# Optimization experiments

Hardware: AMD Instinct MI355X
Metric: run time of the kernel (lower is better)

Reference implementation:

```python
import jax, jax.numpy as jnp
import numpy as np

SIMPLE_W = 1.0
NON_SIMPLE_W = 5.0

# connectivity offset sets (exclude center)
_ALL26 = [(a, b, c) for a in (-1, 0, 1) for b in (-1, 0, 1) for c in (-1, 0, 1) if (a, b, c) != (0, 0, 0)]
OFF6 = [o for o in _ALL26 if abs(o[0]) + abs(o[1]) + abs(o[2]) == 1]          # scipy default structure
OFF18 = [o for o in _ALL26 if not (abs(o[0]) == 1 and abs(o[1]) == 1 and abs(o[2]) == 1)]  # the 's' structure
OFF26 = _ALL26                                                                  # np.ones((3,3,3))


def global_label(fg):
    """Connected-component labels (6-connectivity) via max-propagation.
    Labels are distinct positive ints per component (values differ from scipy's
    1..K but only label *equality* is used downstream). fg: bool [D,H,W]."""
    D, H, W = fg.shape
    idx = (jnp.arange(fg.size, dtype=jnp.int32) + 1).reshape(fg.shape)
    lab0 = jnp.where(fg, idx, 0)

    def step(lab):
        p = jnp.pad(lab, 1)
        m = lab
        for dz, dy, dx in OFF6:
            m = jnp.maximum(m, p[1 + dz:1 + dz + D, 1 + dy:1 + dy + H, 1 + dx:1 + dx + W])
        return jnp.where(fg, m, 0)

    def cond(c):
        return ~c[1]

    def body(c):
        lab, _ = c
        new = step(lab)
        return new, jnp.all(new == lab)

    lab, _ = jax.lax.while_loop(cond, body, (lab0, jnp.array(False)))
    return lab


def local_ncomp(mask, offsets):
    """Number of connected components inside each 3x3x3 window.
    mask: bool [N,3,3,3]. Max-propagation of unique seeds for 26 iters
    (>= max path length among 27 voxels); a component is counted where the
    surviving max label equals its own seed."""
    seed = (jnp.arange(27, dtype=jnp.int32) + 1).reshape(3, 3, 3)
    lab0 = jnp.where(mask, seed, 0)

    def body(_, lab):
        p = jnp.pad(lab, ((0, 0), (1, 1), (1, 1), (1, 1)))
        m = lab
        for dz, dy, dx in offsets:
            m = jnp.maximum(m, p[:, 1 + dz:4 + dz, 1 + dy:4 + dy, 1 + dx:4 + dx])
        return jnp.where(mask, m, 0)

    lab = jax.lax.fori_loop(0, 26, body, lab0)
    return jnp.sum((lab == seed) & mask, axis=(1, 2, 3))


def nonsimple_map(x):
    """Per-voxel non-simple-point indicator, float, same shape as x."""
    D, H, W = x.shape
    fg = x > 0
    glab = global_label(fg)
    p = jnp.pad(glab, 1, mode='edge')  # np.pad(..., 'edge')
    # 3x3x3 label windows per voxel -> [N,3,3,3]
    wins = jnp.stack([p[dz:dz + D, dy:dy + H, dx:dx + W]
                      for dz in range(3) for dy in range(3) for dx in range(3)], axis=-1)
    wins = wins.reshape(-1, 3, 3, 3)
    center = wins[:, 1, 1, 1]  # [N]
    c = center[:, None, None, None]
    # test 1: complement-of-center-label components (18-connectivity) must be exactly 1
    n1 = local_ncomp(wins != c, OFF18)
    # test 2: center-label components with center voxel removed (26-conn) must be exactly 1
    mask2 = (wins == c).at[:, 1, 1, 1].set(False)
    n2 = local_ncomp(mask2, OFF26)
    ns = (center != 0) & ((n1 != 1) | (n2 != 1))
    return ns.reshape(D, H, W).astype(x.dtype)


def setup_inputs() -> dict:
    key = jax.random.key(0)
    k1, k2 = jax.random.split(key)
    D = H = W = 64
    prediction = jax.random.normal(k1, (D, H, W), dtype=jnp.float32)
    label = jax.random.randint(k2, (D, H, W), 0, 2).astype(jnp.float32)
    return {"prediction": prediction, "label": label}


def reference(prediction, label):
    pw = nonsimple_map(prediction)
    lw = nonsimple_map(label)
    w_bool = (pw + lw) > 0
    weight = jnp.where(w_bool, NON_SIMPLE_W, SIMPLE_W).astype(prediction.dtype)
    # BCEWithLogitsLoss(reduction='none'): max(x,0) - x*y + log(1+exp(-|x|))
    cost = jnp.maximum(prediction, 0.0) - prediction * label + jnp.log1p(jnp.exp(-jnp.abs(prediction)))
    return jnp.mean(weight * cost)
```

## Files before the change

kernel.cpp:

```cpp
#include <hip/hip_runtime.h>

#define DIM 64
#define NVOX (DIM * DIM * DIM)

__device__ __forceinline__ int find_root_link(int* L, int v) {
    for (;;) {
        int p = L[v];
        if (p == v) return v;
        int gp = L[p];
        if (gp == p) return p;
        L[v] = gp;
        v = gp;
    }
}

__device__ __forceinline__ void unite(int* L, int a, int b) {
    int ra = find_root_link(L, a);
    int rb = find_root_link(L, b);
    while (ra != rb) {
        if (ra > rb) { int t = ra; ra = rb; rb = t; }
        int old = atomicCAS(&L[rb], rb, ra);
        if (old == rb) break;
        rb = find_root_link(L, old);
        ra = find_root_link(L, ra);
    }
}

__global__ void local_ccl(const float* __restrict__ pred,
                          const float* __restrict__ lab,
                          int* __restrict__ LP, int* __restrict__ LL) {
    __shared__ int s_lab[512];
    int t = threadIdx.x;
    int b = blockIdx.x;
    int tx = b & 3, ty = (b >> 2) & 7, tz = b >> 5;
    int lx = t & 15, ly = (t >> 4) & 7, lz = t >> 7;
    int x = (tx << 4) | lx, y = (ty << 3) | ly, z = (tz << 2) | lz;
    int v = (z << 12) | (y << 6) | x;

    const float* src = blockIdx.y ? lab : pred;
    int* Lg = blockIdx.y ? LL : LP;

    bool fg = src[v] > 0.0f;
    s_lab[t] = fg ? t : -1;
    __syncthreads();

    if (fg) {
        if (lx < 15 && s_lab[t + 1]   >= 0) unite(s_lab, t, t + 1);
        if (ly < 7  && s_lab[t + 16]  >= 0) unite(s_lab, t, t + 16);
        if (lz < 3  && s_lab[t + 128] >= 0) unite(s_lab, t, t + 128);
    }
    __syncthreads();

    int g = -1;
    if (fg) {
        int p = s_lab[t];
        while (s_lab[p] != p) p = s_lab[p];
        int rx = (tx << 4) | (p & 15);
        int ry = (ty << 3) | ((p >> 4) & 7);
        int rz = (tz << 2) | (p >> 7);
        g = (rz << 12) | (ry << 6) | rx;
    }
    Lg[v] = g;
}

__global__ void boundary_link(int* __restrict__ LP, int* __restrict__ LL) {
    int v = blockIdx.x * blockDim.x + threadIdx.x;
    int x = v & 63, y = (v >> 6) & 63, z = v >> 12;
    bool bx = ((x & 15) == 15) && (x != 63);
    bool by = ((y & 7)  == 7)  && (y != 63);
    bool bz = ((z & 3)  == 3)  && (z != 63);
    if (!(bx | by | bz)) return;
    if (LP[v] >= 0) {
        if (bx && LP[v + 1]    >= 0) unite(LP, v, v + 1);
        if (by && LP[v + 64]   >= 0) unite(LP, v, v + 64);
        if (bz && LP[v + 4096] >= 0) unite(LP, v, v + 4096);
    }
    if (LL[v] >= 0) {
        if (bx && LL[v + 1]    >= 0) unite(LL, v, v + 1);
        if (by && LL[v + 64]   >= 0) unite(LL, v, v + 64);
        if (bz && LL[v + 4096] >= 0) unite(LL, v, v + 4096);
    }
}

__global__ void compress_kernel(int* __restrict__ LP, int* __restrict__ LL) {
    int v = blockIdx.x * blockDim.x + threadIdx.x;
    int p = LP[v];
    if (p >= 0) { int q = LP[p]; while (q != p) { p = q; q = LP[p]; } LP[v] = p; }
    p = LL[v];
    if (p >= 0) { int q = LL[p]; while (q != p) { p = q; q = LL[p]; } LL[v] = p; }
}

#define MX_L 0x6DB6DB6u
#define MX_R 0x36DB6DBu
#define MY_L 0x7E3F1F8u
#define MY_R 0x0FC7E3Fu
#define M27  0x7FFFFFFu

__device__ __forceinline__ unsigned dil26(unsigned m) {
    m |= ((m << 1) & MX_L) | ((m >> 1) & MX_R);
    m |= ((m << 3) & MY_L) | ((m >> 3) & MY_R);
    m |= ((m << 9) & M27)  | (m >> 9);
    return m;
}
__device__ __forceinline__ unsigned dil18(unsigned m) {
    unsigned ax = m | ((m << 1) & MX_L) | ((m >> 1) & MX_R);
    unsigned ay = m | ((m << 3) & MY_L) | ((m >> 3) & MY_R);
    unsigned dxy = ax | ((ax << 3) & MY_L) | ((ax >> 3) & MY_R);
    unsigned dxz = ax | ((ax << 9) & M27)  | (ax >> 9);
    unsigned dyz = ay | ((ay << 9) & M27)  | (ay >> 9);
    return dxy | dxz | dyz;
}

__device__ __forceinline__ bool single18(unsigned m) {
    if (!m) return false;
    unsigned c = m & (~m + 1u);
    for (;;) {
        unsigned n = dil18(c) & m;
        if (n == m) return true;
        if (n == c) return false;
        c = n;
    }
}
__device__ __forceinline__ bool single26(unsigned m) {
    if (!m) return false;
    unsigned c = m & (~m + 1u);
    for (;;) {
        unsigned n = dil26(c) & m;
        if (n == m) return true;
        if (n == c) return false;
        c = n;
    }
}

#define HV 600

__global__ void finalize_kernel(const float* __restrict__ pred,
                                const float* __restrict__ lab,
                                const int* __restrict__ LP,
                                const int* __restrict__ LL,
                                float* __restrict__ out) {
    __shared__ int sP[HV], sL[HV];
    __shared__ float s_part[4];
    int t = threadIdx.x;
    int b = blockIdx.x;
    int tx = b & 7, ty = (b >> 3) & 7, tz = b >> 6;
    int x0 = tx << 3, y0 = ty << 3, z0 = tz << 2;

    for (int i = t; i < HV; i += 256) {
        int hx = i % 10, r = i / 10, hy = r % 10, hz = r / 10;
        int gx = x0 + hx - 1; gx = gx < 0 ? 0 : (gx > 63 ? 63 : gx);
        int gy = y0 + hy - 1; gy = gy < 0 ? 0 : (gy > 63 ? 63 : gy);
        int gz = z0 + hz - 1; gz = gz < 0 ? 0 : (gz > 63 ? 63 : gz);
        int gv = (gz << 12) | (gy << 6) | gx;
        sP[i] = LP[gv];
        sL[i] = LL[gv];
    }
    __syncthreads();

    int lx = t & 7, ly = (t >> 3) & 7, lz = t >> 6;
    int x = x0 | lx, y = y0 | ly, z = z0 | lz;
    int v = (z << 12) | (y << 6) | x;
    int base = lz * 100 + ly * 10 + lx;

    bool nsP = false, nsL = false;
    {
        int c = sP[base + 111];
        if (c >= 0) {
            unsigned m1 = 0, m2 = 0; int k = 0;
#pragma unroll
            for (int kz = 0; kz < 3; ++kz)
#pragma unroll
                for (int ky = 0; ky < 3; ++ky)
#pragma unroll
                    for (int kx = 0; kx < 3; ++kx, ++k) {
                        int w = sP[base + kz * 100 + ky * 10 + kx];
                        m1 |= (unsigned)(w != c) << k;
                        m2 |= (unsigned)(w == c) << k;
                    }
            m2 &= ~(1u << 13);
            nsP = !(single18(m1) && single26(m2));
        }
    }
    {
        int c = sL[base + 111];
        if (c >= 0) {
            unsigned m1 = 0, m2 = 0; int k = 0;
#pragma unroll
            for (int kz = 0; kz < 3; ++kz)
#pragma unroll
                for (int ky = 0; ky < 3; ++ky)
#pragma unroll
                    for (int kx = 0; kx < 3; ++kx, ++k) {
                        int w = sL[base + kz * 100 + ky * 10 + kx];
                        m1 |= (unsigned)(w != c) << k;
                        m2 |= (unsigned)(w == c) << k;
                    }
            m2 &= ~(1u << 13);
            nsL = !(single18(m1) && single26(m2));
        }
    }

    float p = pred[v], l = lab[v];
    float cost = fmaxf(p, 0.0f) - p * l + log1pf(__expf(-fabsf(p)));
    float w = (nsP || nsL) ? 5.0f : 1.0f;
    float contrib = w * cost;

#pragma unroll
    for (int off = 32; off > 0; off >>= 1)
        contrib += __shfl_down(contrib, off, 64);
    if ((t & 63) == 0) s_part[t >> 6] = contrib;
    __syncthreads();
    if (t == 0) {
        float s = s_part[0] + s_part[1] + s_part[2] + s_part[3];
        atomicAdd(out, s * (1.0f / (float)NVOX));
    }
}

extern "C" void kernel_launch(void* const* d_in, const int* in_sizes, int n_in,
                              void* d_out, int out_size, void* d_ws, size_t ws_size,
                              hipStream_t stream) {
    const float* pred = (const float*)d_in[0];
    const float* lab  = (const float*)d_in[1];
    float* out = (float*)d_out;

    int* LP = (int*)d_ws;
    int* LL = LP + NVOX;

    hipMemsetAsync(d_out, 0, sizeof(float), stream);

    hipLaunchKernelGGL(local_ccl, dim3(512, 2), dim3(512), 0, stream,
                       pred, lab, LP, LL);
    hipLaunchKernelGGL(boundary_link, dim3(NVOX / 256), dim3(256), 0, stream,
                       LP, LL);
    hipLaunchKernelGGL(compress_kernel, dim3(NVOX / 256), dim3(256), 0, stream,
                       LP, LL);
    hipLaunchKernelGGL(finalize_kernel, dim3(NVOX / 256), dim3(256), 0, stream,
                       pred, lab, LP, LL, out);
}
```

Baseline: 128.1 us.

## Enlarge CCL tiles, index boundary edges directly, fold root compression into finalize

Local CCL tiles grow from 16x8x4 to 16x16x8 voxels, with each thread handling 8 voxels, so far fewer inter-tile boundary edges remain. The boundary kernel now enumerates only the actual boundary face pairs, one edge per thread, instead of scanning every voxel and exiting early. The separate compress kernel is removed, and finalize chases each halo voxel's chain to its root while loading it. This cuts one launch and most idle boundary threads, but finalize now performs uncompressed pointer chasing for every halo element, which can be deep chains of global reads.

```diff
diff --git a/kernel.cpp b/kernel.cpp
--- a/kernel.cpp
+++ b/kernel.cpp
@@ -29,65 +29,79 @@
 __global__ void local_ccl(const float* __restrict__ pred,
                           const float* __restrict__ lab,
                           int* __restrict__ LP, int* __restrict__ LL) {
-    __shared__ int s_lab[512];
+    __shared__ int s_lab[2048];
     int t = threadIdx.x;
     int b = blockIdx.x;
-    int tx = b & 3, ty = (b >> 2) & 7, tz = b >> 5;
-    int lx = t & 15, ly = (t >> 4) & 7, lz = t >> 7;
-    int x = (tx << 4) | lx, y = (ty << 3) | ly, z = (tz << 2) | lz;
-    int v = (z << 12) | (y << 6) | x;
+    int tx = b & 3, ty = (b >> 2) & 3, tz = b >> 4;
+    int X0 = tx << 4, Y0 = ty << 4, Z0 = tz << 3;
 
     const float* src = blockIdx.y ? lab : pred;
     int* Lg = blockIdx.y ? LL : LP;
 
-    bool fg = src[v] > 0.0f;
-    s_lab[t] = fg ? t : -1;
-    __syncthreads();
-
-    if (fg) {
-        if (lx < 15 && s_lab[t + 1]   >= 0) unite(s_lab, t, t + 1);
-        if (ly < 7  && s_lab[t + 16]  >= 0) unite(s_lab, t, t + 16);
-        if (lz < 3  && s_lab[t + 128] >= 0) unite(s_lab, t, t + 128);
-    }
-    __syncthreads();
-
-    int g = -1;
-    if (fg) {
-        int p = s_lab[t];
-        while (s_lab[p] != p) p = s_lab[p];
-        int rx = (tx << 4) | (p & 15);
-        int ry = (ty << 3) | ((p >> 4) & 7);
-        int rz = (tz << 2) | (p >> 7);
-        g = (rz << 12) | (ry << 6) | rx;
-    }
-    Lg[v] = g;
-}
+    bool fg[8];
+    int vv[8];
+#pragma unroll
+    for (int i = 0; i < 8; ++i) {
+        int l = t + (i << 8);
+        int v = ((Z0 + (l >> 8)) << 12) | ((Y0 + ((l >> 4) & 15)) << 6)
+              | (X0 + (l & 15));
+        vv[i] = v;
+        fg[i] = src[v] > 0.0f;
+        s_lab[l] = fg[i] ? l : -1;
+    }
+    __syncthreads();
+
+#pragma unroll
+    for (int i = 0; i < 8; ++i) {
+        if (!fg[i]) continue;
+        int l = t + (i << 8);
+        int lx = l & 15, ly = (l >> 4) & 15, lz = l >> 8;
+        if (lx < 15 && s_lab[l + 1]   >= 0) unite(s_lab, l, l + 1);
+        if (ly < 15 && s_lab[l + 16]  >= 0) unite(s_lab, l, l + 16);
+        if (lz < 7  && s_lab[l + 256] >= 0) unite(s_lab, l, l + 256);
+    }
+    __syncthreads();
+
+#pragma unroll
+    for (int i = 0; i < 8; ++i) {
+        int g = -1;
+        if (fg[i]) {
+            int p = s_lab[t + (i << 8)];
+            while (s_lab[p] != p) p = s_lab[p];
+            g = ((Z0 + (p >> 8)) << 12) | ((Y0 + ((p >> 4) & 15)) << 6)
+              | (X0 + (p & 15));
+        }
+        Lg[vv[i]] = g;
+    }
+}
+
+#define EPF 53248
 
 __global__ void boundary_link(int* __restrict__ LP, int* __restrict__ LL) {
-    int v = blockIdx.x * blockDim.x + threadIdx.x;
-    int x = v & 63, y = (v >> 6) & 63, z = v >> 12;
-    bool bx = ((x & 15) == 15) && (x != 63);
-    bool by = ((y & 7)  == 7)  && (y != 63);
-    bool bz = ((z & 3)  == 3)  && (z != 63);
-    if (!(bx | by | bz)) return;
-    if (LP[v] >= 0) {
-        if (bx && LP[v + 1]    >= 0) unite(LP, v, v + 1);
-        if (by && LP[v + 64]   >= 0) unite(LP, v, v + 64);
-        if (bz && LP[v + 4096] >= 0) unite(LP, v, v + 4096);
-    }
-    if (LL[v] >= 0) {
-        if (bx && LL[v + 1]    >= 0) unite(LL, v, v + 1);
-        if (by && LL[v + 64]   >= 0) unite(LL, v, v + 64);
-        if (bz && LL[v + 4096] >= 0) unite(LL, v, v + 4096);
-    }
-}
-
-__global__ void compress_kernel(int* __restrict__ LP, int* __restrict__ LL) {
-    int v = blockIdx.x * blockDim.x + threadIdx.x;
-    int p = LP[v];
-    if (p >= 0) { int q = LP[p]; while (q != p) { p = q; q = LP[p]; } LP[v] = p; }
-    p = LL[v];
-    if (p >= 0) { int q = LL[p]; while (q != p) { p = q; q = LL[p]; } LL[v] = p; }
+    int e = blockIdx.x * blockDim.x + threadIdx.x;
+    int f = e >= EPF;
+    int r = f ? e - EPF : e;
+    int* L = f ? LL : LP;
+    int v, n;
+    if (r < 12288) {
+        int plane = 15 + ((r >> 12) << 4);
+        int ij = r & 4095;
+        v = ((ij >> 6) << 12) | ((ij & 63) << 6) | plane;
+        n = v + 1;
+    } else if (r < 24576) {
+        int r2 = r - 12288;
+        int plane = 15 + ((r2 >> 12) << 4);
+        int ij = r2 & 4095;
+        v = ((ij >> 6) << 12) | (plane << 6) | (ij & 63);
+        n = v + 64;
+    } else {
+        int r3 = r - 24576;
+        int plane = 7 + ((r3 >> 12) << 3);
+        int ij = r3 & 4095;
+        v = (plane << 12) | ((ij >> 6) << 6) | (ij & 63);
+        n = v + 4096;
+    }
+    if (L[v] >= 0 && L[n] >= 0) unite(L, v, n);
 }
 
 #define MX_L 0x6DB6DB6u
@@ -152,8 +166,12 @@
         int gy = y0 + hy - 1; gy = gy < 0 ? 0 : (gy > 63 ? 63 : gy);
         int gz = z0 + hz - 1; gz = gz < 0 ? 0 : (gz > 63 ? 63 : gz);
         int gv = (gz << 12) | (gy << 6) | gx;
-        sP[i] = LP[gv];
-        sL[i] = LL[gv];
+        int p = LP[gv];
+        if (p >= 0) { int q = LP[p]; while (q != p) { p = q; q = LP[p]; } }
+        sP[i] = p;
+        p = LL[gv];
+        if (p >= 0) { int q = LL[p]; while (q != p) { p = q; q = LL[p]; } }
+        sL[i] = p;
     }
     __syncthreads();
 
@@ -228,11 +246,9 @@
 
     hipMemsetAsync(d_out, 0, sizeof(float), stream);
 
-    hipLaunchKernelGGL(local_ccl, dim3(512, 2), dim3(512), 0, stream,
+    hipLaunchKernelGGL(local_ccl, dim3(128, 2), dim3(256), 0, stream,
                        pred, lab, LP, LL);
-    hipLaunchKernelGGL(boundary_link, dim3(NVOX / 256), dim3(256), 0, stream,
-                       LP, LL);
-    hipLaunchKernelGGL(compress_kernel, dim3(NVOX / 256), dim3(256), 0, stream,
+    hipLaunchKernelGGL(boundary_link, dim3(2 * EPF / 256), dim3(256), 0, stream,
                        LP, LL);
     hipLaunchKernelGGL(finalize_kernel, dim3(NVOX / 256), dim3(256), 0, stream,
                        pred, lab, LP, LL, out);
```

Result: faster. 116.0 us (-9.4%).
